# Performance work log

Measured on AMD Instinct MI355X. Metric: run time of the kernel, lower is better.

## Reference

```python
import jax, jax.numpy as jnp
import numpy as np

B, H, N, C = 1024, 768, 100000, 42
LABELED_WEIGHT = 0.7
NUM_LABELED = 100000  # used verbatim in (1 - num_labeled) per the original source
EPS = 1e-8  # F.cosine_similarity default eps


def setup_inputs() -> dict:
    key = jax.random.key(0)
    k1, k2, k3, k4 = jax.random.split(key, 4)
    return {
        "weak_data": jax.random.normal(k1, (B, H), dtype=jnp.float32),
        "weak_logits": jax.random.normal(k2, (B, C), dtype=jnp.float32),
        "labeled_memory": jax.random.normal(k3, (N, H), dtype=jnp.float32),
        "labeled_logits": jax.random.normal(k4, (N, C), dtype=jnp.float32),
    }


def reference(weak_data, weak_logits, labeled_memory, labeled_logits):
    # cosine similarity: normalize rows with eps-clamped norms, then one GEMM
    dn = weak_data / jnp.maximum(jnp.linalg.norm(weak_data, axis=-1, keepdims=True), EPS)
    mn = labeled_memory / jnp.maximum(jnp.linalg.norm(labeled_memory, axis=-1, keepdims=True), EPS)
    sim = jnp.einsum("bh,nh->bn", dn, mn)  # [B, N] similarity (the large intermediate)
    ids = jnp.argmax(sim, axis=1)          # 1-NN index per batch row
    batch_logits = labeled_logits[ids]     # gather [B, C]
    # faithful to source: coefficient is (1 - num_labeled), as written in update_logits
    return batch_logits * LABELED_WEIGHT + (1.0 - NUM_LABELED) * weak_logits
```

## Files before the change

kernel.cpp:

```cpp
#include <hip/hip_runtime.h>
#include <stdint.h>

#define B_ROWS 1024
#define H_DIM  768
#define N_ROWS 100000
#define C_DIM  42
#define NB     32
#define NCHUNK 3125
#define NP     64
#define NY     8

typedef __attribute__((ext_vector_type(4))) float f32x4;
typedef unsigned long long ull;

__device__ __forceinline__ ull packvi(float v, unsigned n) {
    unsigned u = __float_as_uint(v);
    u = (u & 0x80000000u) ? ~u : (u | 0x80000000u);
    return ((ull)u << 32) | (ull)(~n);
}

__device__ __forceinline__ int pk8(float4 v) {
    int d = __builtin_amdgcn_cvt_pk_fp8_f32(v.x, v.y, 0, false);
    d     = __builtin_amdgcn_cvt_pk_fp8_f32(v.z, v.w, d, true);
    return d;
}

__device__ __forceinline__ int swz(int k, int kg, int n) {
    return (k * 1024 + kg * 256 + n * 8) ^ ((kg << 3) | ((k & 3) << 5));
}

__global__ void k_convA(const float* __restrict__ wd, int2* __restrict__ A2) {
    int g = blockIdx.x * 256 + threadIdx.x;
    int row = g / 96;
    int rem = g - row * 96;
    int k = rem >> 2, kgrp = rem & 3;
    const float* s = wd + row * H_DIM + k * 32 + kgrp * 8;
    float4 v0 = *reinterpret_cast<const float4*>(s);
    float4 v1 = *reinterpret_cast<const float4*>(s + 4);
    int rg = row >> 4, fr = row & 15;
    A2[((rg * 24 + k) * 64 + kgrp * 16 + fr)] = make_int2(pk8(v0), pk8(v1));
}

__global__ __launch_bounds__(256, 2) void k_simmax(
    const float* __restrict__ mem,
    const long* __restrict__ A2,
    ull* __restrict__ partial)
{
    __shared__ __align__(16) char ldsB[2][24 * 1024];
    __shared__ float ldsS[4][NB];

    const int t    = threadIdx.x;
    const int lane = t & 63;
    const int wv   = t >> 6;
    const int fr   = lane & 15;
    const int kgrp = lane >> 4;
    const int bx   = blockIdx.x;
    const int y    = bx >> 6;
    const int p    = bx & 63;

    const int RG0 = y * 8 + wv * 2;
    long Afr[2][24];
    #pragma unroll
    for (int rg = 0; rg < 2; ++rg) {
        const long* ap = A2 + (size_t)(RG0 + rg) * 24 * 64 + lane;
        #pragma unroll
        for (int k = 0; k < 24; ++k) Afr[rg][k] = ap[k * 64];
    }

    float    bv[2][2][4];
    unsigned bi[2][2][4];
    #pragma unroll
    for (int rg = 0; rg < 2; ++rg)
        #pragma unroll
        for (int nt = 0; nt < 2; ++nt)
            #pragma unroll
            for (int r = 0; r < 4; ++r) { bv[rg][nt][r] = -1e30f; bi[rg][nt][r] = 0u; }

    const int nc = (p < 53) ? 49 : 48;

    auto stage = [&](int c, int bb, int ns) {
        #pragma unroll 4
        for (int uu = 0; uu < 12; ++uu) {
            int ug = t + 256 * uu;
            int n  = ug / 96;
            int rm = ug - n * 96;
            int k = rm >> 2, kg = rm & 3;
            const float* s = mem + (size_t)(c * NB + n) * H_DIM + k * 32 + kg * 8;
            float4 v0 = *reinterpret_cast<const float4*>(s);
            float4 v1 = *reinterpret_cast<const float4*>(s + 4);
            float ss = v0.x*v0.x + v0.y*v0.y + v0.z*v0.z + v0.w*v0.w
                     + v1.x*v1.x + v1.y*v1.y + v1.z*v1.z + v1.w*v1.w;
            atomicAdd(&ldsS[ns][n], ss);
            *reinterpret_cast<int2*>(&ldsB[bb][swz(k, kg, n)]) =
                make_int2(pk8(v0), pk8(v1));
        }
    };

    if (t < NB) { ldsS[0][t] = 0.f; ldsS[1][t] = 0.f; }
    __syncthreads();
    stage(p, 0, 0);

    for (int i = 0; i < nc; ++i) {
        __syncthreads();
        if (t < NB) ldsS[(i + 2) & 3][t] = 0.f;
        if (i + 1 < nc) stage(p + (i + 1) * NP, (i + 1) & 1, (i + 1) & 3);

        const int c  = p + i * NP;
        const int bb = i & 1;
        const int ns = i & 3;

        f32x4 acc[2][2];
        #pragma unroll
        for (int rg = 0; rg < 2; ++rg)
            #pragma unroll
            for (int nt = 0; nt < 2; ++nt)
                acc[rg][nt] = (f32x4){0.f, 0.f, 0.f, 0.f};

        #pragma unroll
        for (int k = 0; k < 24; ++k) {
            long bfr0 = *reinterpret_cast<const long*>(&ldsB[bb][swz(k, kgrp, fr)]);
            long bfr1 = *reinterpret_cast<const long*>(&ldsB[bb][swz(k, kgrp, 16 + fr)]);
            #pragma unroll
            for (int rg = 0; rg < 2; ++rg) {
                acc[rg][0] = __builtin_amdgcn_mfma_f32_16x16x32_fp8_fp8(Afr[rg][k], bfr0, acc[rg][0], 0, 0, 0);
                acc[rg][1] = __builtin_amdgcn_mfma_f32_16x16x32_fp8_fp8(Afr[rg][k], bfr1, acc[rg][1], 0, 0, 0);
            }
        }

        float inv0 = __frsqrt_rn(fmaxf(ldsS[ns][fr],      1e-16f));
        float inv1 = __frsqrt_rn(fmaxf(ldsS[ns][16 + fr], 1e-16f));
        const unsigned n0 = (unsigned)(c * NB) + (unsigned)fr;
        #pragma unroll
        for (int rg = 0; rg < 2; ++rg)
            #pragma unroll
            for (int r = 0; r < 4; ++r) {
                float v0 = acc[rg][0][r] * inv0;
                float v1 = acc[rg][1][r] * inv1;
                bool p0 = v0 > bv[rg][0][r];
                bv[rg][0][r] = p0 ? v0 : bv[rg][0][r];
                bi[rg][0][r] = p0 ? n0 : bi[rg][0][r];
                bool p1 = v1 > bv[rg][1][r];
                bv[rg][1][r] = p1 ? v1 : bv[rg][1][r];
                bi[rg][1][r] = p1 ? (n0 + 16) : bi[rg][1][r];
            }
    }

    #pragma unroll
    for (int rg = 0; rg < 2; ++rg)
        #pragma unroll
        for (int r = 0; r < 4; ++r) {
            ull P0 = packvi(bv[rg][0][r], bi[rg][0][r]);
            ull P1 = packvi(bv[rg][1][r], bi[rg][1][r]);
            ull P  = (P1 > P0) ? P1 : P0;
            #pragma unroll
            for (int s = 1; s < 16; s <<= 1) {
                ull o = __shfl_xor(P, s);
                P = (o > P) ? o : P;
            }
            if (fr == 0) {
                int b = y * 128 + wv * 32 + rg * 16 + kgrp * 4 + r;
                partial[(size_t)p * B_ROWS + b] = P;
            }
        }
}

__global__ void k_final(const ull* __restrict__ partial,
                        const float* __restrict__ wlog,
                        const float* __restrict__ llog,
                        float* __restrict__ out)
{
    const int t    = threadIdx.x;
    const int lane = t & 63;
    const int wv   = t >> 6;
    const int b    = blockIdx.x * 4 + wv;

    ull P = partial[(size_t)lane * B_ROWS + b];
    #pragma unroll
    for (int s = 1; s < 64; s <<= 1) {
        ull o = __shfl_xor(P, s);
        P = (o > P) ? o : P;
    }
    int idx = (int)(~(unsigned)(P & 0xFFFFFFFFull));
    if (lane < C_DIM)
        out[b * C_DIM + lane] = 0.7f * llog[(size_t)idx * C_DIM + lane]
                              - 99999.0f * wlog[b * C_DIM + lane];
}

extern "C" void kernel_launch(void* const* d_in, const int* in_sizes, int n_in,
                              void* d_out, int out_size, void* d_ws, size_t ws_size,
                              hipStream_t stream) {
    const float* weak_data   = (const float*)d_in[0];
    const float* weak_logits = (const float*)d_in[1];
    const float* mem         = (const float*)d_in[2];
    const float* llog        = (const float*)d_in[3];
    float* out = (float*)d_out;

    int2* A2      = (int2*)d_ws;
    ull*  partial = (ull*)((char*)d_ws + 0x100000);

    k_convA <<<384, 256, 0, stream>>>(weak_data, A2);
    k_simmax<<<NY * NP, 256, 0, stream>>>(mem, (const long*)A2, partial);
    k_final <<<256, 256, 0, stream>>>(partial, weak_logits, llog, out);
}
```

Baseline: 922.7 us.

## Precompute memory row norms and overlap global prefetch with split MFMA phases

Adds a separate kernel that computes inverse L2 norms of all memory rows, so the main kernel no longer does LDS atomic adds while staging. The main loop now loads the next chunk into registers in two halves, interleaved with the two halves of the MFMA k-loop, and writes them to the other LDS buffer afterwards. This aims to hide global-load latency behind matrix math and to cut the barriers per iteration. In exchange, the memory matrix is read one extra time and register pressure rises from the staging registers.

```diff
diff --git a/kernel.cpp b/kernel.cpp
--- a/kernel.cpp
+++ b/kernel.cpp
@@ -6,7 +6,6 @@
 #define N_ROWS 100000
 #define C_DIM  42
 #define NB     32
-#define NCHUNK 3125
 #define NP     64
 #define NY     8
 
@@ -27,6 +26,21 @@
 
 __device__ __forceinline__ int swz(int k, int kg, int n) {
     return (k * 1024 + kg * 256 + n * 8) ^ ((kg << 3) | ((k & 3) << 5));
+}
+
+__global__ void k_norms(const float* __restrict__ mem, float* __restrict__ inrm) {
+    int w    = (blockIdx.x * 256 + threadIdx.x) >> 6;
+    int lane = threadIdx.x & 63;
+    const float4* src = reinterpret_cast<const float4*>(mem + (size_t)w * H_DIM) + lane;
+    float ss = 0.f;
+    #pragma unroll
+    for (int j = 0; j < 3; ++j) {
+        float4 v = src[j * 64];
+        ss += v.x*v.x + v.y*v.y + v.z*v.z + v.w*v.w;
+    }
+    #pragma unroll
+    for (int s = 1; s < 64; s <<= 1) ss += __shfl_xor(ss, s);
+    if (lane == 0) inrm[w] = 1.0f / fmaxf(sqrtf(ss), 1e-8f);
 }
 
 __global__ void k_convA(const float* __restrict__ wd, int2* __restrict__ A2) {
@@ -43,20 +57,19 @@
 
 __global__ __launch_bounds__(256, 2) void k_simmax(
     const float* __restrict__ mem,
-    const long* __restrict__ A2,
+    const long*  __restrict__ A2,
+    const float* __restrict__ inrm,
     ull* __restrict__ partial)
 {
     __shared__ __align__(16) char ldsB[2][24 * 1024];
-    __shared__ float ldsS[4][NB];
 
     const int t    = threadIdx.x;
     const int lane = t & 63;
     const int wv   = t >> 6;
     const int fr   = lane & 15;
     const int kgrp = lane >> 4;
-    const int bx   = blockIdx.x;
-    const int y    = bx >> 6;
-    const int p    = bx & 63;
+    const int y    = blockIdx.x >> 6;
+    const int p    = blockIdx.x & 63;
 
     const int RG0 = y * 8 + wv * 2;
     long Afr[2][24];
@@ -78,36 +91,44 @@
 
     const int nc = (p < 53) ? 49 : 48;
 
-    auto stage = [&](int c, int bb, int ns) {
-        #pragma unroll 4
-        for (int uu = 0; uu < 12; ++uu) {
-            int ug = t + 256 * uu;
-            int n  = ug / 96;
-            int rm = ug - n * 96;
-            int k = rm >> 2, kg = rm & 3;
-            const float* s = mem + (size_t)(c * NB + n) * H_DIM + k * 32 + kg * 8;
-            float4 v0 = *reinterpret_cast<const float4*>(s);
-            float4 v1 = *reinterpret_cast<const float4*>(s + 4);
-            float ss = v0.x*v0.x + v0.y*v0.y + v0.z*v0.z + v0.w*v0.w
-                     + v1.x*v1.x + v1.y*v1.y + v1.z*v1.z + v1.w*v1.w;
-            atomicAdd(&ldsS[ns][n], ss);
-            *reinterpret_cast<int2*>(&ldsB[bb][swz(k, kg, n)]) =
-                make_int2(pk8(v0), pk8(v1));
-        }
-    };
-
-    if (t < NB) { ldsS[0][t] = 0.f; ldsS[1][t] = 0.f; }
+
+    #pragma unroll
+    for (int uu = 0; uu < 12; ++uu) {
+        int ug = t + 256 * uu;
+        int n = ug / 96, rm = ug - n * 96;
+        const float* s = mem + (size_t)p * (NB * H_DIM) + n * H_DIM + rm * 8;
+        float4 v0 = *reinterpret_cast<const float4*>(s);
+        float4 v1 = *reinterpret_cast<const float4*>(s + 4);
+        *reinterpret_cast<int2*>(&ldsB[0][swz(rm >> 2, rm & 3, n)]) =
+            make_int2(pk8(v0), pk8(v1));
+    }
+    float inv0 = inrm[p * NB + fr];
+    float inv1 = inrm[p * NB + 16 + fr];
     __syncthreads();
-    stage(p, 0, 0);
 
     for (int i = 0; i < nc; ++i) {
-        __syncthreads();
-        if (t < NB) ldsS[(i + 2) & 3][t] = 0.f;
-        if (i + 1 < nc) stage(p + (i + 1) * NP, (i + 1) & 1, (i + 1) & 3);
-
-        const int c  = p + i * NP;
-        const int bb = i & 1;
-        const int ns = i & 3;
+        const int  c   = p + i * NP;
+        const int  cur = i & 1;
+        const bool pf  = (i + 1 < nc);
+        const size_t nbase = (size_t)(c + NP) * (NB * H_DIM);
+
+        float4 st[12];
+        if (pf) {
+            #pragma unroll
+            for (int uu = 0; uu < 6; ++uu) {
+                int ug = t + 256 * uu;
+                int n = ug / 96, rm = ug - n * 96;
+                const float* s = mem + nbase + n * H_DIM + rm * 8;
+                st[2 * uu]     = *reinterpret_cast<const float4*>(s);
+                st[2 * uu + 1] = *reinterpret_cast<const float4*>(s + 4);
+            }
+        }
+        float ninv0 = 0.f, ninv1 = 0.f;
+        if (pf) {
+            ninv0 = inrm[(c + NP) * NB + fr];
+            ninv1 = inrm[(c + NP) * NB + 16 + fr];
+        }
+        __builtin_amdgcn_sched_barrier(0);
 
         f32x4 acc[2][2];
         #pragma unroll
@@ -117,18 +138,56 @@
                 acc[rg][nt] = (f32x4){0.f, 0.f, 0.f, 0.f};
 
         #pragma unroll
-        for (int k = 0; k < 24; ++k) {
-            long bfr0 = *reinterpret_cast<const long*>(&ldsB[bb][swz(k, kgrp, fr)]);
-            long bfr1 = *reinterpret_cast<const long*>(&ldsB[bb][swz(k, kgrp, 16 + fr)]);
-            #pragma unroll
-            for (int rg = 0; rg < 2; ++rg) {
-                acc[rg][0] = __builtin_amdgcn_mfma_f32_16x16x32_fp8_fp8(Afr[rg][k], bfr0, acc[rg][0], 0, 0, 0);
-                acc[rg][1] = __builtin_amdgcn_mfma_f32_16x16x32_fp8_fp8(Afr[rg][k], bfr1, acc[rg][1], 0, 0, 0);
-            }
-        }
-
-        float inv0 = __frsqrt_rn(fmaxf(ldsS[ns][fr],      1e-16f));
-        float inv1 = __frsqrt_rn(fmaxf(ldsS[ns][16 + fr], 1e-16f));
+        for (int k = 0; k < 12; ++k) {
+            long b0 = *reinterpret_cast<const long*>(&ldsB[cur][swz(k, kgrp, fr)]);
+            long b1 = *reinterpret_cast<const long*>(&ldsB[cur][swz(k, kgrp, 16 + fr)]);
+            acc[0][0] = __builtin_amdgcn_mfma_f32_16x16x32_fp8_fp8(Afr[0][k], b0, acc[0][0], 0, 0, 0);
+            acc[0][1] = __builtin_amdgcn_mfma_f32_16x16x32_fp8_fp8(Afr[0][k], b1, acc[0][1], 0, 0, 0);
+            acc[1][0] = __builtin_amdgcn_mfma_f32_16x16x32_fp8_fp8(Afr[1][k], b0, acc[1][0], 0, 0, 0);
+            acc[1][1] = __builtin_amdgcn_mfma_f32_16x16x32_fp8_fp8(Afr[1][k], b1, acc[1][1], 0, 0, 0);
+        }
+        __builtin_amdgcn_sched_barrier(0);
+
+        if (pf) {
+            #pragma unroll
+            for (int uu = 0; uu < 6; ++uu) {
+                int ug = t + 256 * uu;
+                int n = ug / 96, rm = ug - n * 96;
+                *reinterpret_cast<int2*>(&ldsB[cur ^ 1][swz(rm >> 2, rm & 3, n)]) =
+                    make_int2(pk8(st[2 * uu]), pk8(st[2 * uu + 1]));
+            }
+            #pragma unroll
+            for (int uu = 6; uu < 12; ++uu) {
+                int ug = t + 256 * uu;
+                int n = ug / 96, rm = ug - n * 96;
+                const float* s = mem + nbase + n * H_DIM + rm * 8;
+                st[2 * (uu - 6)]     = *reinterpret_cast<const float4*>(s);
+                st[2 * (uu - 6) + 1] = *reinterpret_cast<const float4*>(s + 4);
+            }
+        }
+        __builtin_amdgcn_sched_barrier(0);
+
+        #pragma unroll
+        for (int k = 12; k < 24; ++k) {
+            long b0 = *reinterpret_cast<const long*>(&ldsB[cur][swz(k, kgrp, fr)]);
+            long b1 = *reinterpret_cast<const long*>(&ldsB[cur][swz(k, kgrp, 16 + fr)]);
+            acc[0][0] = __builtin_amdgcn_mfma_f32_16x16x32_fp8_fp8(Afr[0][k], b0, acc[0][0], 0, 0, 0);
+            acc[0][1] = __builtin_amdgcn_mfma_f32_16x16x32_fp8_fp8(Afr[0][k], b1, acc[0][1], 0, 0, 0);
+            acc[1][0] = __builtin_amdgcn_mfma_f32_16x16x32_fp8_fp8(Afr[1][k], b0, acc[1][0], 0, 0, 0);
+            acc[1][1] = __builtin_amdgcn_mfma_f32_16x16x32_fp8_fp8(Afr[1][k], b1, acc[1][1], 0, 0, 0);
+        }
+        __builtin_amdgcn_sched_barrier(0);
+
+        if (pf) {
+            #pragma unroll
+            for (int uu = 6; uu < 12; ++uu) {
+                int ug = t + 256 * uu;
+                int n = ug / 96, rm = ug - n * 96;
+                *reinterpret_cast<int2*>(&ldsB[cur ^ 1][swz(rm >> 2, rm & 3, n)]) =
+                    make_int2(pk8(st[2 * (uu - 6)]), pk8(st[2 * (uu - 6) + 1]));
+            }
+        }
+
         const unsigned n0 = (unsigned)(c * NB) + (unsigned)fr;
         #pragma unroll
         for (int rg = 0; rg < 2; ++rg)
@@ -143,6 +202,8 @@
                 bv[rg][1][r] = p1 ? v1 : bv[rg][1][r];
                 bi[rg][1][r] = p1 ? (n0 + 16) : bi[rg][1][r];
             }
+        inv0 = ninv0; inv1 = ninv1;
+        __syncthreads();
     }
 
     #pragma unroll
@@ -195,10 +256,12 @@
     const float* llog        = (const float*)d_in[3];
     float* out = (float*)d_out;
 
-    int2* A2      = (int2*)d_ws;
-    ull*  partial = (ull*)((char*)d_ws + 0x100000);
-
+    int2*  A2      = (int2*)d_ws;
+    float* inrm    = (float*)((char*)d_ws + 0xC0000);
+    ull*   partial = (ull*)((char*)d_ws + 0x140000);
+
+    k_norms <<<25000, 256, 0, stream>>>(mem, inrm);
     k_convA <<<384, 256, 0, stream>>>(weak_data, A2);
-    k_simmax<<<NY * NP, 256, 0, stream>>>(mem, (const long*)A2, partial);
+    k_simmax<<<NY * NP, 256, 0, stream>>>(mem, (const long*)A2, inrm, partial);
     k_final <<<256, 256, 0, stream>>>(partial, weak_logits, llog, out);
 }
```

Result: slower. 969.7 us (+5.1%).
